# Kernel optimization log

Measured on AMD Instinct MI355X. Metric: run time of the kernel, lower is better.

Reference implementation:

```python
import jax, jax.numpy as jnp
import numpy as np

N = 50000          # nodes
E = 800000         # edges (before self-loops)
G = 64             # graphs in batch
VOCAB = 10000
EMB = 62
HEADS = 4
C = 64             # per-head channels
NUM_CLASSES = 10
NEG_SLOPE = 0.2


def setup_inputs() -> dict:
    key = jax.random.key(0)
    ks = jax.random.split(key, 24)
    inp = {}
    inp['x_ids'] = jax.random.randint(ks[0], (N,), 0, VOCAB)
    inp['degrees'] = jax.random.uniform(ks[1], (N, 2), dtype=jnp.float32)
    inp['edge_src'] = jax.random.randint(ks[2], (E,), 0, N)
    inp['edge_dst'] = jax.random.randint(ks[3], (E,), 0, N)
    inp['batch'] = jnp.sort(jax.random.randint(ks[4], (N,), 0, G))
    # parameters
    inp['emb'] = jax.random.normal(ks[5], (VOCAB, EMB), dtype=jnp.float32)
    d_in = EMB + 2  # 64
    s = lambda f: 1.0 / np.sqrt(f)
    inp['W1'] = jax.random.normal(ks[6], (HEADS * C, d_in), dtype=jnp.float32) * s(d_in)
    inp['as1'] = jax.random.normal(ks[7], (HEADS, C), dtype=jnp.float32) * s(C)
    inp['ad1'] = jax.random.normal(ks[8], (HEADS, C), dtype=jnp.float32) * s(C)
    inp['b1'] = jnp.zeros((HEADS * C,), dtype=jnp.float32)
    inp['W2'] = jax.random.normal(ks[9], (HEADS * C, HEADS * C), dtype=jnp.float32) * s(HEADS * C)
    inp['as2'] = jax.random.normal(ks[10], (HEADS, C), dtype=jnp.float32) * s(C)
    inp['ad2'] = jax.random.normal(ks[11], (HEADS, C), dtype=jnp.float32) * s(C)
    inp['b2'] = jnp.zeros((HEADS * C,), dtype=jnp.float32)
    inp['W3'] = jax.random.normal(ks[12], (1 * C, HEADS * C), dtype=jnp.float32) * s(HEADS * C)
    inp['as3'] = jax.random.normal(ks[13], (1, C), dtype=jnp.float32) * s(C)
    inp['ad3'] = jax.random.normal(ks[14], (1, C), dtype=jnp.float32) * s(C)
    inp['b3'] = jnp.zeros((C,), dtype=jnp.float32)
    inp['linW'] = jax.random.normal(ks[15], (NUM_CLASSES, C), dtype=jnp.float32) * s(C)
    inp['linb'] = jnp.zeros((NUM_CLASSES,), dtype=jnp.float32)
    return inp


def gat_conv(x, src, dst, W, att_src, att_dst, bias, heads, out_ch, concat):
    n = x.shape[0]
    h = (x @ W.T).reshape(n, heads, out_ch)              # [N,H,C]
    a_src = jnp.sum(h * att_src, axis=-1)                # [N,H]
    a_dst = jnp.sum(h * att_dst, axis=-1)                # [N,H]
    e = jax.nn.leaky_relu(a_src[src] + a_dst[dst], NEG_SLOPE)  # [E,H]
    # segmented softmax over incoming edges of each dst node
    emax = jax.ops.segment_max(e, dst, num_segments=n)
    ex = jnp.exp(e - emax[dst])
    denom = jax.ops.segment_sum(ex, dst, num_segments=n)
    alpha = ex / (denom[dst] + 1e-16)                    # [E,H]
    msg = h[src] * alpha[:, :, None]                     # [E,H,C]
    out = jax.ops.segment_sum(msg, dst, num_segments=n)  # [N,H,C]
    out = out.reshape(n, heads * out_ch) if concat else out.mean(axis=1)
    return out + bias


def reference(x_ids, degrees, edge_src, edge_dst, batch, emb,
              W1, as1, ad1, b1, W2, as2, ad2, b2, W3, as3, ad3, b3, linW, linb):
    n = x_ids.shape[0]
    # add self-loops (PyG GATConv default)
    loop = jnp.arange(n)
    src = jnp.concatenate([edge_src, loop])
    dst = jnp.concatenate([edge_dst, loop])
    x = jnp.concatenate([emb[x_ids], degrees], axis=1)   # [N, EMB+2]
    x = jax.nn.relu(gat_conv(x, src, dst, W1, as1, ad1, b1, HEADS, C, True))
    x = jax.nn.relu(gat_conv(x, src, dst, W2, as2, ad2, b2, HEADS, C, True))
    x = jax.nn.relu(gat_conv(x, src, dst, W3, as3, ad3, b3, 1, C, False))
    # global mean pool over graphs
    sums = jax.ops.segment_sum(x, batch, num_segments=G)                    # [G,C]
    cnts = jax.ops.segment_sum(jnp.ones((n,), x.dtype), batch, num_segments=G)
    pooled = sums / jnp.maximum(cnts, 1.0)[:, None]
    return pooled @ linW.T + linb                         # [G, num_classes]
```

## Files before the change

kernel.cpp:

```cpp
#include <hip/hip_runtime.h>
#include <hip/hip_bf16.h>
#include <cstdint>

#define NEG_SLOPE 0.2f

typedef __bf16 bf16x8 __attribute__((ext_vector_type(8)));
typedef float  f32x4  __attribute__((ext_vector_type(4)));

__device__ __forceinline__ unsigned short f2bf(float f) {
    unsigned int u = __float_as_uint(f);
    u += 0x7fffu + ((u >> 16) & 1u);
    return (unsigned short)(u >> 16);
}
__device__ __forceinline__ float bf2f(unsigned short u) {
    return __uint_as_float((unsigned int)u << 16);
}

__global__ void prep_kernel(const float* __restrict__ W1, int n1,
                            const float* __restrict__ W2, int n2,
                            const float* __restrict__ W3, int n3,
                            unsigned short* __restrict__ w1b, unsigned short* __restrict__ w2b,
                            unsigned short* __restrict__ w3b,
                            const int* __restrict__ ids, const float* __restrict__ degs,
                            const float* __restrict__ emb, unsigned short* __restrict__ x,
                            const int* __restrict__ edst, int* __restrict__ cnt,
                            const int* __restrict__ batch, int* __restrict__ gcnt,
                            int Nn, int E0, int E2, int G,
                            int bW, int bX, int bH)
{
    int b = blockIdx.x;
    if (b < bW) {
        int i = b * 256 + threadIdx.x;
        if (i < n1) w1b[i] = f2bf(W1[i]);
        int j = i - n1;
        if (j >= 0 && j < n2) w2b[j] = f2bf(W2[j]);
        int k = j - n2;
        if (k >= 0 && k < n3) w3b[k] = f2bf(W3[k]);
    } else if (b < bX) {
        int node = (b - bW) * 4 + (threadIdx.x >> 6);
        int lane = threadIdx.x & 63;
        if (node < Nn) {
            int id = ids[node];
            float v;
            if (lane < 62) v = emb[(size_t)id * 62 + lane];
            else           v = degs[node * 2 + (lane - 62)];
            x[(size_t)node * 64 + lane] = f2bf(v);
        }
    } else if (b < bH) {
        int e = (b - bX) * 256 + threadIdx.x;
        if (e < E2) {
            int d = (e < E0) ? edst[e] : (e - E0);
            atomicAdd(&cnt[d], 1);
        }
    } else {
        int g = threadIdx.x;
        if (g < G) {
            int lo0 = 0, hi = Nn;
            while (lo0 < hi) { int mid = (lo0 + hi) >> 1; if (batch[mid] < g) lo0 = mid + 1; else hi = mid; }
            int lo1 = lo0; hi = Nn;
            while (lo1 < hi) { int mid = (lo1 + hi) >> 1; if (batch[mid] < g + 1) lo1 = mid + 1; else hi = mid; }
            gcnt[g] = lo1 - lo0;
        }
    }
}

__global__ void scan_part_kernel(const int* __restrict__ cnt, int* __restrict__ part, int Nn)
{
    int t = threadIdx.x;
    int base = blockIdx.x * 2048 + t * 8;
    int s = 0;
    if (base + 8 <= Nn) {
        int4 a = *reinterpret_cast<const int4*>(cnt + base);
        int4 b = *reinterpret_cast<const int4*>(cnt + base + 4);
        s = a.x + a.y + a.z + a.w + b.x + b.y + b.z + b.w;
    } else {
        for (int k = 0; k < 8; ++k)
            if (base + k < Nn) s += cnt[base + k];
    }
#pragma unroll
    for (int off = 32; off >= 1; off >>= 1) s += __shfl_xor(s, off, 64);
    __shared__ int ws[4];
    int wid = t >> 6;
    if ((t & 63) == 0) ws[wid] = s;
    __syncthreads();
    if (t == 0) part[blockIdx.x] = ws[0] + ws[1] + ws[2] + ws[3];
}

__global__ void scan_top_kernel(int* __restrict__ part, int nparts)
{
    int t = threadIdx.x;
    int v = (t < nparts) ? part[t] : 0;
    int orig = v;
#pragma unroll
    for (int off = 1; off <= 32; off <<= 1) {
        int u = __shfl_up(v, off, 64);
        if (t >= off) v += u;
    }
    if (t < nparts) part[t] = v - orig;
}

__global__ void scan_down_kernel(const int* __restrict__ cnt, const int* __restrict__ part,
                                 int* __restrict__ row_off, int* __restrict__ cursor,
                                 int Nn, int total)
{
    int t = threadIdx.x;
    int base = blockIdx.x * 2048 + t * 8;
    int v[8];
    if (base + 8 <= Nn) {
        int4 a = *reinterpret_cast<const int4*>(cnt + base);
        int4 b = *reinterpret_cast<const int4*>(cnt + base + 4);
        v[0]=a.x; v[1]=a.y; v[2]=a.z; v[3]=a.w; v[4]=b.x; v[5]=b.y; v[6]=b.z; v[7]=b.w;
    } else {
#pragma unroll
        for (int k = 0; k < 8; ++k) v[k] = (base + k < Nn) ? cnt[base + k] : 0;
    }
    int tsum = 0;
#pragma unroll
    for (int k = 0; k < 8; ++k) tsum += v[k];
    int incl = tsum;
#pragma unroll
    for (int off = 1; off <= 32; off <<= 1) {
        int u = __shfl_up(incl, off, 64);
        if ((t & 63) >= off) incl += u;
    }
    int texcl = incl - tsum;
    __shared__ int ws[4];
    int wid = t >> 6;
    if ((t & 63) == 63) ws[wid] = incl;
    __syncthreads();
    int wbase = 0;
#pragma unroll
    for (int w = 0; w < 4; ++w) wbase += (w < wid) ? ws[w] : 0;
    int run = part[blockIdx.x] + wbase + texcl;

    if (base + 8 <= Nn) {
        int o[8];
#pragma unroll
        for (int k = 0; k < 8; ++k) { o[k] = run; run += v[k]; }
        *reinterpret_cast<int4*>(row_off + base)     = make_int4(o[0], o[1], o[2], o[3]);
        *reinterpret_cast<int4*>(row_off + base + 4) = make_int4(o[4], o[5], o[6], o[7]);
        *reinterpret_cast<int4*>(cursor + base)      = make_int4(o[0], o[1], o[2], o[3]);
        *reinterpret_cast<int4*>(cursor + base + 4)  = make_int4(o[4], o[5], o[6], o[7]);
    } else {
#pragma unroll
        for (int k = 0; k < 8; ++k) {
            if (base + k < Nn) {
                row_off[base + k] = run;
                cursor[base + k]  = run;
                run += v[k];
            }
        }
    }
    if (blockIdx.x == 0 && t == 0) row_off[Nn] = total;
}

__global__ void scatter_kernel(const int* __restrict__ esrc, const int* __restrict__ edst,
                               int* __restrict__ cursor, int* __restrict__ csr_src,
                               int E0, int E2)
{
    int e = blockIdx.x * blockDim.x + threadIdx.x;
    if (e >= E2) return;
    int s, d;
    if (e < E0) { s = esrc[e]; d = edst[e]; }
    else        { s = d = e - E0; }
    int pos = atomicAdd(&cursor[d], 1);
    csr_src[pos] = s;
}

__global__ void gemm_mfma(const unsigned short* __restrict__ X, const unsigned short* __restrict__ Wb,
                          unsigned short* __restrict__ Hout,
                          const float* __restrict__ aSrc, const float* __restrict__ aDst,
                          float* __restrict__ a_s, float* __restrict__ a_d,
                          int Nn, int K, int F)
{
    int wid  = (blockIdx.x * blockDim.x + threadIdx.x) >> 6;
    int lane = threadIdx.x & 63;
    int mtiles = (Nn + 63) >> 6;
    int ftiles = F >> 6;
    if (wid >= mtiles * ftiles) return;
    int ft = wid / mtiles;
    int mt = wid - ft * mtiles;
    int m0 = mt << 6, f0 = ft << 6;
    int r = lane & 15, g = lane >> 4, g4 = g << 2;

    const unsigned short* xrow[4];
#pragma unroll
    for (int ja = 0; ja < 4; ++ja) {
        int row = m0 + ja * 16 + r;
        if (row >= Nn) row = Nn - 1;
        xrow[ja] = X + (size_t)row * K + g * 8;
    }
    const unsigned short* wrow = Wb + (size_t)(f0 + r) * K + g * 8;
    const size_t wstep = (size_t)16 * K;

    f32x4 acc[4][4];
#pragma unroll
    for (int a = 0; a < 4; ++a)
#pragma unroll
        for (int b = 0; b < 4; ++b) acc[a][b] = f32x4{0.f, 0.f, 0.f, 0.f};

    for (int k0 = 0; k0 < K; k0 += 32) {
        bf16x8 av[4], bv[4];
#pragma unroll
        for (int ja = 0; ja < 4; ++ja) av[ja] = *reinterpret_cast<const bf16x8*>(xrow[ja] + k0);
#pragma unroll
        for (int jb = 0; jb < 4; ++jb) bv[jb] = *reinterpret_cast<const bf16x8*>(wrow + jb * wstep + k0);
#pragma unroll
        for (int ja = 0; ja < 4; ++ja)
#pragma unroll
            for (int jb = 0; jb < 4; ++jb)
                acc[ja][jb] = __builtin_amdgcn_mfma_f32_16x16x32_bf16(av[ja], bv[jb], acc[ja][jb], 0, 0, 0);
    }

#pragma unroll
    for (int ja = 0; ja < 4; ++ja)
#pragma unroll
        for (int q = 0; q < 4; ++q) {
            int row = m0 + ja * 16 + g4 + q;
            if (row < Nn) {
#pragma unroll
                for (int jb = 0; jb < 4; ++jb)
                    Hout[(size_t)row * F + f0 + jb * 16 + r] = f2bf(acc[ja][jb][q]);
            }
        }

    float ps[4][4], pd[4][4];
#pragma unroll
    for (int ja = 0; ja < 4; ++ja)
#pragma unroll
        for (int q = 0; q < 4; ++q) { ps[ja][q] = 0.f; pd[ja][q] = 0.f; }
#pragma unroll
    for (int jb = 0; jb < 4; ++jb) {
        float ws_ = aSrc[f0 + jb * 16 + r];
        float wd_ = aDst[f0 + jb * 16 + r];
#pragma unroll
        for (int ja = 0; ja < 4; ++ja)
#pragma unroll
            for (int q = 0; q < 4; ++q) {
                ps[ja][q] += acc[ja][jb][q] * ws_;
                pd[ja][q] += acc[ja][jb][q] * wd_;
            }
    }
#pragma unroll
    for (int off = 1; off < 16; off <<= 1)
#pragma unroll
        for (int ja = 0; ja < 4; ++ja)
#pragma unroll
            for (int q = 0; q < 4; ++q) {
                ps[ja][q] += __shfl_xor(ps[ja][q], off, 64);
                pd[ja][q] += __shfl_xor(pd[ja][q], off, 64);
            }
    if (r == 0) {
        int Hh = F >> 6;
#pragma unroll
        for (int ja = 0; ja < 4; ++ja)
#pragma unroll
            for (int q = 0; q < 4; ++q) {
                int n = m0 + ja * 16 + g4 + q;
                if (n < Nn) {
                    a_s[(size_t)n * Hh + ft] = ps[ja][q];
                    a_d[(size_t)n * Hh + ft] = pd[ja][q];
                }
            }
    }
}

template<int H>
__global__ void aggregate_kernel(const unsigned short* __restrict__ Hb,
                                 const float* __restrict__ a_s, const float* __restrict__ a_d,
                                 const int* __restrict__ row_off, const int* __restrict__ csr_src,
                                 const float* __restrict__ bias,
                                 unsigned short* __restrict__ out, int Nn)
{
    constexpr int F = H * 64;
    constexpr int VEC = F / 64;
    __shared__ int   s_sn[4][64];
    __shared__ float s_e[4][64][H];
    int w = threadIdx.x >> 6;
    int node = blockIdx.x * 4 + w;
    int lane = threadIdx.x & 63;
    if (node >= Nn) return;
    int start = row_off[node], end = row_off[node + 1];
    int deg = end - start;

    float adn[H];
#pragma unroll
    for (int h = 0; h < H; ++h) adn[h] = a_d[(size_t)node * H + h];

    if (deg <= 64) {
        bool act = lane < deg;
        int sn = act ? csr_src[start + lane] : 0;
        float v[H];
        if (H == 4) {
            const f32x4 av = *reinterpret_cast<const f32x4*>(a_s + (size_t)sn * 4);
#pragma unroll
            for (int h = 0; h < 4; ++h) {
                float t = av[h] + adn[h];
                t = (t > 0.f) ? t : NEG_SLOPE * t;
                v[h] = act ? t : -1e30f;
            }
        } else {
            float t = a_s[sn] + adn[0];
            t = (t > 0.f) ? t : NEG_SLOPE * t;
            v[0] = act ? t : -1e30f;
        }
        float m[H], e[H], s[H];
#pragma unroll
        for (int h = 0; h < H; ++h) {
            m[h] = v[h];
#pragma unroll
            for (int off = 32; off >= 1; off >>= 1)
                m[h] = fmaxf(m[h], __shfl_xor(m[h], off, 64));
        }
#pragma unroll
        for (int h = 0; h < H; ++h) {
            e[h] = act ? __expf(v[h] - m[h]) : 0.f;
            s[h] = e[h];
#pragma unroll
            for (int off = 32; off >= 1; off >>= 1)
                s[h] += __shfl_xor(s[h], off, 64);
        }

        s_sn[w][lane] = sn;
#pragma unroll
        for (int h = 0; h < H; ++h) s_e[w][lane][h] = e[h];
        asm volatile("s_waitcnt lgkmcnt(0)" ::: "memory");

        if (H == 4) {
            int half = lane >> 5, laneh = lane & 31, hd = laneh >> 3;
            float acc[8];
#pragma unroll
            for (int k = 0; k < 8; ++k) acc[k] = 0.f;
            for (int j = 0; j < deg; j += 2) {
                int idx = j + half;
                int snj = s_sn[w][idx];
                float ex = s_e[w][idx][hd];
                const uint4 u = *reinterpret_cast<const uint4*>(Hb + (size_t)snj * 256 + laneh * 8);
                acc[0] += ex * __uint_as_float(u.x << 16);
                acc[1] += ex * __uint_as_float(u.x & 0xffff0000u);
                acc[2] += ex * __uint_as_float(u.y << 16);
                acc[3] += ex * __uint_as_float(u.y & 0xffff0000u);
                acc[4] += ex * __uint_as_float(u.z << 16);
                acc[5] += ex * __uint_as_float(u.z & 0xffff0000u);
                acc[6] += ex * __uint_as_float(u.w << 16);
                acc[7] += ex * __uint_as_float(u.w & 0xffff0000u);
            }
#pragma unroll
            for (int k = 0; k < 8; ++k) acc[k] += __shfl_xor(acc[k], 32, 64);
            if (lane < 32) {
                float sh = (hd == 0) ? s[0] : (hd == 1) ? s[1] : (hd == 2) ? s[2] : s[3];
                float inv = 1.f / (sh + 1e-16f);
                unsigned int pk[4];
#pragma unroll
                for (int k = 0; k < 4; ++k) {
                    float t0 = acc[2*k]   * inv + bias[laneh * 8 + 2*k];
                    float t1 = acc[2*k+1] * inv + bias[laneh * 8 + 2*k + 1];
                    unsigned int lo = f2bf(t0 > 0.f ? t0 : 0.f);
                    unsigned int hi = f2bf(t1 > 0.f ? t1 : 0.f);
                    pk[k] = lo | (hi << 16);
                }
                *reinterpret_cast<uint4*>(out + (size_t)node * 256 + laneh * 8) =
                    make_uint4(pk[0], pk[1], pk[2], pk[3]);
            }
        } else {
            int qtr = lane >> 4, laneq = lane & 15;
            float acc[4];
#pragma unroll
            for (int k = 0; k < 4; ++k) acc[k] = 0.f;
            for (int j = 0; j < deg; j += 4) {
                int idx = j + qtr;
                int snj = s_sn[w][idx];
                float ex = s_e[w][idx][0];
                const uint2 u = *reinterpret_cast<const uint2*>(Hb + (size_t)snj * 64 + laneq * 4);
                acc[0] += ex * __uint_as_float(u.x << 16);
                acc[1] += ex * __uint_as_float(u.x & 0xffff0000u);
                acc[2] += ex * __uint_as_float(u.y << 16);
                acc[3] += ex * __uint_as_float(u.y & 0xffff0000u);
            }
#pragma unroll
            for (int k = 0; k < 4; ++k) {
                acc[k] += __shfl_xor(acc[k], 32, 64);
                acc[k] += __shfl_xor(acc[k], 16, 64);
            }
            if (lane < 16) {
                float inv = 1.f / (s[0] + 1e-16f);
                unsigned int pk[2];
#pragma unroll
                for (int k = 0; k < 2; ++k) {
                    float t0 = acc[2*k]   * inv + bias[laneq * 4 + 2*k];
                    float t1 = acc[2*k+1] * inv + bias[laneq * 4 + 2*k + 1];
                    unsigned int lo = f2bf(t0 > 0.f ? t0 : 0.f);
                    unsigned int hi = f2bf(t1 > 0.f ? t1 : 0.f);
                    pk[k] = lo | (hi << 16);
                }
                *reinterpret_cast<uint2*>(out + (size_t)node * 64 + laneq * 4) =
                    make_uint2(pk[0], pk[1]);
            }
        }
        return;
    }

    int head = (H == 1) ? 0 : (lane >> 4);
    float m[H], s[H];
#pragma unroll
    for (int h = 0; h < H; ++h) { m[h] = -1e30f; s[h] = 0.f; }
    for (int j = start + lane; j < end; j += 64) {
        int sn = csr_src[j];
#pragma unroll
        for (int h = 0; h < H; ++h) {
            float t = a_s[(size_t)sn * H + h] + adn[h];
            t = (t > 0.f) ? t : NEG_SLOPE * t;
            m[h] = fmaxf(m[h], t);
        }
    }
#pragma unroll
    for (int off = 32; off >= 1; off >>= 1)
#pragma unroll
        for (int h = 0; h < H; ++h) m[h] = fmaxf(m[h], __shfl_xor(m[h], off, 64));
    for (int j = start + lane; j < end; j += 64) {
        int sn = csr_src[j];
#pragma unroll
        for (int h = 0; h < H; ++h) {
            float t = a_s[(size_t)sn * H + h] + adn[h];
            t = (t > 0.f) ? t : NEG_SLOPE * t;
            s[h] += __expf(t - m[h]);
        }
    }
#pragma unroll
    for (int off = 32; off >= 1; off >>= 1)
#pragma unroll
        for (int h = 0; h < H; ++h) s[h] += __shfl_xor(s[h], off, 64);

    float mh, sh, adh;
    if (H == 1) { mh = m[0]; sh = s[0]; adh = adn[0]; }
    else {
        mh  = (head == 0) ? m[0]   : (head == 1) ? m[1]   : (head == 2) ? m[2]   : m[3];
        sh  = (head == 0) ? s[0]   : (head == 1) ? s[1]   : (head == 2) ? s[2]   : s[3];
        adh = (head == 0) ? adn[0] : (head == 1) ? adn[1] : (head == 2) ? adn[2] : adn[3];
    }
    float inv = 1.f / (sh + 1e-16f);
    float acc[VEC];
#pragma unroll
    for (int k = 0; k < VEC; ++k) acc[k] = 0.f;
    for (int j = start; j < end; ++j) {
        int sn = csr_src[j];
        float t = a_s[(size_t)sn * H + head] + adh;
        t = (t > 0.f) ? t : NEG_SLOPE * t;
        float ex = __expf(t - mh);
        const unsigned short* hp = Hb + (size_t)sn * F + lane * VEC;
#pragma unroll
        for (int k = 0; k < VEC; ++k) acc[k] += ex * bf2f(hp[k]);
    }
#pragma unroll
    for (int k = 0; k < VEC; ++k) {
        int f = lane * VEC + k;
        float t = acc[k] * inv + bias[f];
        out[(size_t)node * F + f] = f2bf(t > 0.f ? t : 0.f);
    }
}

__global__ void pool_kernel(const unsigned short* __restrict__ x, const int* __restrict__ batch,
                            float* __restrict__ gsums, int Nn)
{
    int lane = threadIdx.x;
    int n0 = blockIdx.x * 64;
    if (n0 >= Nn) return;
    int nend = min(n0 + 64, Nn);
    float acc = 0.f;
    int gcur = batch[n0];
    for (int n = n0; n < nend; ++n) {
        int g = batch[n];
        if (g != gcur) {
            atomicAdd(&gsums[gcur * 64 + lane], acc);
            acc = 0.f;
            gcur = g;
        }
        acc += bf2f(x[(size_t)n * 64 + lane]);
    }
    atomicAdd(&gsums[gcur * 64 + lane], acc);
}

__global__ void final_kernel(const float* __restrict__ gsums, const int* __restrict__ gcnt,
                             const float* __restrict__ linW, const float* __restrict__ linb,
                             float* __restrict__ out, int G)
{
    int t = threadIdx.x;
    if (t >= G * 10) return;
    int g = t / 10, j = t % 10;
    float cnt = (float)max(gcnt[g], 1);
    float acc = 0.f;
#pragma unroll
    for (int c = 0; c < 64; ++c) acc += gsums[g * 64 + c] * linW[j * 64 + c];
    out[g * 10 + j] = acc / cnt + linb[j];
}

extern "C" void kernel_launch(void* const* d_in, const int* in_sizes, int n_in,
                              void* d_out, int out_size, void* d_ws, size_t ws_size,
                              hipStream_t stream)
{
    const int*   x_ids    = (const int*)d_in[0];
    const float* degrees  = (const float*)d_in[1];
    const int*   edge_src = (const int*)d_in[2];
    const int*   edge_dst = (const int*)d_in[3];
    const int*   batch    = (const int*)d_in[4];
    const float* emb      = (const float*)d_in[5];
    const float* W1  = (const float*)d_in[6];
    const float* as1 = (const float*)d_in[7];
    const float* ad1 = (const float*)d_in[8];
    const float* b1  = (const float*)d_in[9];
    const float* W2  = (const float*)d_in[10];
    const float* as2 = (const float*)d_in[11];
    const float* ad2 = (const float*)d_in[12];
    const float* b2  = (const float*)d_in[13];
    const float* W3  = (const float*)d_in[14];
    const float* as3 = (const float*)d_in[15];
    const float* ad3 = (const float*)d_in[16];
    const float* b3  = (const float*)d_in[17];
    const float* linW = (const float*)d_in[18];
    const float* linb = (const float*)d_in[19];

    const int N  = in_sizes[0];
    const int E0 = in_sizes[2];
    const int E2 = E0 + N;
    const int G  = out_size / 10;
    const int nW1 = in_sizes[6], nW2 = in_sizes[10], nW3 = in_sizes[14];

    char* p = (char*)d_ws;
    size_t off = 0;
    auto take = [&](size_t bytes) {
        void* q = p + off;
        off = (off + bytes + 255) & ~(size_t)255;
        return q;
    };
    unsigned short* xA  = (unsigned short*)take((size_t)N * 256 * 2);
    unsigned short* xB  = (unsigned short*)take((size_t)N * 256 * 2);
    float* a_s     = (float*)take((size_t)N * 4 * 4);
    float* a_d     = (float*)take((size_t)N * 4 * 4);
    int*   cnt     = (int*)take((size_t)N * 4);
    int*   row_off = (int*)take((size_t)(N + 1) * 4);
    int*   cursor  = (int*)take((size_t)N * 4);
    int*   csr_src = (int*)take((size_t)E2 * 4);
    float* gsums   = (float*)take((size_t)G * 64 * 4);
    int*   gcnt    = (int*)take((size_t)G * 4);
    int*   part    = (int*)take((size_t)64 * 4);
    unsigned short* w1b = (unsigned short*)take((size_t)nW1 * 2);
    unsigned short* w2b = (unsigned short*)take((size_t)nW2 * 2);
    unsigned short* w3b = (unsigned short*)take((size_t)nW3 * 2);

    hipMemsetAsync(cnt, 0, (size_t)N * 4, stream);
    hipMemsetAsync(gsums, 0, (size_t)G * 64 * 4, stream);

    const int nodeBlocks4 = (N + 3) / 4;
    const int edgeBlocks  = (E2 + 255) / 256;
    const int scanBlocks  = (N + 2047) / 2048;

    const int nWtot = nW1 + nW2 + nW3;
    const int bW = (nWtot + 255) / 256;
    const int bX = bW + nodeBlocks4;
    const int bH = bX + edgeBlocks;
    prep_kernel<<<bH + 1, 256, 0, stream>>>(W1, nW1, W2, nW2, W3, nW3, w1b, w2b, w3b,
                                            x_ids, degrees, emb, xA,
                                            edge_dst, cnt, batch, gcnt,
                                            N, E0, E2, G, bW, bX, bH);

    scan_part_kernel<<<scanBlocks, 256, 0, stream>>>(cnt, part, N);
    scan_top_kernel<<<1, 64, 0, stream>>>(part, scanBlocks);
    scan_down_kernel<<<scanBlocks, 256, 0, stream>>>(cnt, part, row_off, cursor, N, E2);
    scatter_kernel<<<edgeBlocks, 256, 0, stream>>>(edge_src, edge_dst, cursor, csr_src, E0, E2);

    const int mtiles = (N + 63) / 64;
    auto gemmBlocks = [&](int ftiles) { return (mtiles * ftiles + 3) / 4; };

    gemm_mfma<<<gemmBlocks(4), 256, 0, stream>>>(xA, w1b, xB, as1, ad1, a_s, a_d, N, 64, 256);
    aggregate_kernel<4><<<nodeBlocks4, 256, 0, stream>>>(xB, a_s, a_d, row_off, csr_src, b1, xA, N);
    gemm_mfma<<<gemmBlocks(4), 256, 0, stream>>>(xA, w2b, xB, as2, ad2, a_s, a_d, N, 256, 256);
    aggregate_kernel<4><<<nodeBlocks4, 256, 0, stream>>>(xB, a_s, a_d, row_off, csr_src, b2, xA, N);
    gemm_mfma<<<gemmBlocks(1), 256, 0, stream>>>(xA, w3b, xB, as3, ad3, a_s, a_d, N, 256, 64);
    aggregate_kernel<1><<<nodeBlocks4, 256, 0, stream>>>(xB, a_s, a_d, row_off, csr_src, b3, xA, N);

    pool_kernel<<<(N + 63) / 64, 64, 0, stream>>>(xA, batch, gsums, N);
    final_kernel<<<1, ((G * 10 + 63) / 64) * 64, 0, stream>>>(gsums, gcnt, linW, linb, (float*)d_out, G);
}
```

Baseline: 391.8 us.

## Replace CSR build with fixed 64-slot per-node buckets plus overflow list

Drops the scan and scatter kernels. Edges are now placed directly into fixed 64-entry per-destination buckets during the counting pass, and edges past the 64th go to a global overflow list that high-degree nodes search linearly. The aggregate kernels are also reworked: each lane now loads wider chunks of features (32 bytes for 4 heads, 16 bytes for 1 head), and a packed (source, exp) pair is kept in LDS. This removes four launches and a pass over the edges, at the cost of a larger bucket buffer and a slow linear overflow scan if many nodes exceed 64 edges.

```diff
diff --git a/kernel.cpp b/kernel.cpp
--- a/kernel.cpp
+++ b/kernel.cpp
@@ -14,6 +14,10 @@
 }
 __device__ __forceinline__ float bf2f(unsigned short u) {
     return __uint_as_float((unsigned int)u << 16);
+}
+__device__ __forceinline__ void fma2(float2& a, float ex, unsigned int u) {
+    a.x = fmaf(ex, __uint_as_float(u << 16),         a.x);
+    a.y = fmaf(ex, __uint_as_float(u & 0xffff0000u), a.y);
 }
 
 __global__ void prep_kernel(const float* __restrict__ W1, int n1,
@@ -23,7 +27,9 @@
                             unsigned short* __restrict__ w3b,
                             const int* __restrict__ ids, const float* __restrict__ degs,
                             const float* __restrict__ emb, unsigned short* __restrict__ x,
-                            const int* __restrict__ edst, int* __restrict__ cnt,
+                            const int* __restrict__ esrc, const int* __restrict__ edst,
+                            int* __restrict__ cnt, int* __restrict__ bucket,
+                            int* __restrict__ ovd, int* __restrict__ ovs, int* __restrict__ n_over,
                             const int* __restrict__ batch, int* __restrict__ gcnt,
                             int Nn, int E0, int E2, int G,
                             int bW, int bX, int bH)
@@ -49,8 +55,15 @@
     } else if (b < bH) {
         int e = (b - bX) * 256 + threadIdx.x;
         if (e < E2) {
-            int d = (e < E0) ? edst[e] : (e - E0);
-            atomicAdd(&cnt[d], 1);
+            int s, d;
+            if (e < E0) { s = esrc[e]; d = edst[e]; }
+            else        { s = d = e - E0; }
+            int pos = atomicAdd(&cnt[d], 1);
+            if (pos < 64) bucket[(size_t)d * 64 + pos] = s;
+            else {
+                int o = atomicAdd(n_over, 1);
+                ovd[o] = d; ovs[o] = s;
+            }
         }
     } else {
         int g = threadIdx.x;
@@ -62,109 +75,6 @@
             gcnt[g] = lo1 - lo0;
         }
     }
-}
-
-__global__ void scan_part_kernel(const int* __restrict__ cnt, int* __restrict__ part, int Nn)
-{
-    int t = threadIdx.x;
-    int base = blockIdx.x * 2048 + t * 8;
-    int s = 0;
-    if (base + 8 <= Nn) {
-        int4 a = *reinterpret_cast<const int4*>(cnt + base);
-        int4 b = *reinterpret_cast<const int4*>(cnt + base + 4);
-        s = a.x + a.y + a.z + a.w + b.x + b.y + b.z + b.w;
-    } else {
-        for (int k = 0; k < 8; ++k)
-            if (base + k < Nn) s += cnt[base + k];
-    }
-#pragma unroll
-    for (int off = 32; off >= 1; off >>= 1) s += __shfl_xor(s, off, 64);
-    __shared__ int ws[4];
-    int wid = t >> 6;
-    if ((t & 63) == 0) ws[wid] = s;
-    __syncthreads();
-    if (t == 0) part[blockIdx.x] = ws[0] + ws[1] + ws[2] + ws[3];
-}
-
-__global__ void scan_top_kernel(int* __restrict__ part, int nparts)
-{
-    int t = threadIdx.x;
-    int v = (t < nparts) ? part[t] : 0;
-    int orig = v;
-#pragma unroll
-    for (int off = 1; off <= 32; off <<= 1) {
-        int u = __shfl_up(v, off, 64);
-        if (t >= off) v += u;
-    }
-    if (t < nparts) part[t] = v - orig;
-}
-
-__global__ void scan_down_kernel(const int* __restrict__ cnt, const int* __restrict__ part,
-                                 int* __restrict__ row_off, int* __restrict__ cursor,
-                                 int Nn, int total)
-{
-    int t = threadIdx.x;
-    int base = blockIdx.x * 2048 + t * 8;
-    int v[8];
-    if (base + 8 <= Nn) {
-        int4 a = *reinterpret_cast<const int4*>(cnt + base);
-        int4 b = *reinterpret_cast<const int4*>(cnt + base + 4);
-        v[0]=a.x; v[1]=a.y; v[2]=a.z; v[3]=a.w; v[4]=b.x; v[5]=b.y; v[6]=b.z; v[7]=b.w;
-    } else {
-#pragma unroll
-        for (int k = 0; k < 8; ++k) v[k] = (base + k < Nn) ? cnt[base + k] : 0;
-    }
-    int tsum = 0;
-#pragma unroll
-    for (int k = 0; k < 8; ++k) tsum += v[k];
-    int incl = tsum;
-#pragma unroll
-    for (int off = 1; off <= 32; off <<= 1) {
-        int u = __shfl_up(incl, off, 64);
-        if ((t & 63) >= off) incl += u;
-    }
-    int texcl = incl - tsum;
-    __shared__ int ws[4];
-    int wid = t >> 6;
-    if ((t & 63) == 63) ws[wid] = incl;
-    __syncthreads();
-    int wbase = 0;
-#pragma unroll
-    for (int w = 0; w < 4; ++w) wbase += (w < wid) ? ws[w] : 0;
-    int run = part[blockIdx.x] + wbase + texcl;
-
-    if (base + 8 <= Nn) {
-        int o[8];
-#pragma unroll
-        for (int k = 0; k < 8; ++k) { o[k] = run; run += v[k]; }
-        *reinterpret_cast<int4*>(row_off + base)     = make_int4(o[0], o[1], o[2], o[3]);
-        *reinterpret_cast<int4*>(row_off + base + 4) = make_int4(o[4], o[5], o[6], o[7]);
-        *reinterpret_cast<int4*>(cursor + base)      = make_int4(o[0], o[1], o[2], o[3]);
-        *reinterpret_cast<int4*>(cursor + base + 4)  = make_int4(o[4], o[5], o[6], o[7]);
-    } else {
-#pragma unroll
-        for (int k = 0; k < 8; ++k) {
-            if (base + k < Nn) {
-                row_off[base + k] = run;
-                cursor[base + k]  = run;
-                run += v[k];
-            }
-        }
-    }
-    if (blockIdx.x == 0 && t == 0) row_off[Nn] = total;
-}
-
-__global__ void scatter_kernel(const int* __restrict__ esrc, const int* __restrict__ edst,
-                               int* __restrict__ cursor, int* __restrict__ csr_src,
-                               int E0, int E2)
-{
-    int e = blockIdx.x * blockDim.x + threadIdx.x;
-    if (e >= E2) return;
-    int s, d;
-    if (e < E0) { s = esrc[e]; d = edst[e]; }
-    else        { s = d = e - E0; }
-    int pos = atomicAdd(&cursor[d], 1);
-    csr_src[pos] = s;
 }
 
 __global__ void gemm_mfma(const unsigned short* __restrict__ X, const unsigned short* __restrict__ Wb,
@@ -268,20 +178,20 @@
 template<int H>
 __global__ void aggregate_kernel(const unsigned short* __restrict__ Hb,
                                  const float* __restrict__ a_s, const float* __restrict__ a_d,
-                                 const int* __restrict__ row_off, const int* __restrict__ csr_src,
+                                 const int* __restrict__ cnt, const int* __restrict__ bucket,
+                                 const int* __restrict__ ovd, const int* __restrict__ ovs,
+                                 const int* __restrict__ n_over,
                                  const float* __restrict__ bias,
                                  unsigned short* __restrict__ out, int Nn)
 {
     constexpr int F = H * 64;
     constexpr int VEC = F / 64;
-    __shared__ int   s_sn[4][64];
-    __shared__ float s_e[4][64][H];
+    __shared__ uint2 s_pk[4][64][H];
     int w = threadIdx.x >> 6;
     int node = blockIdx.x * 4 + w;
     int lane = threadIdx.x & 63;
     if (node >= Nn) return;
-    int start = row_off[node], end = row_off[node + 1];
-    int deg = end - start;
+    int deg = cnt[node];
 
     float adn[H];
 #pragma unroll
@@ -289,7 +199,7 @@
 
     if (deg <= 64) {
         bool act = lane < deg;
-        int sn = act ? csr_src[start + lane] : 0;
+        int sn = act ? bucket[(size_t)node * 64 + lane] : 0;
         float v[H];
         if (H == 4) {
             const f32x4 av = *reinterpret_cast<const f32x4*>(a_s + (size_t)sn * 4);
@@ -321,91 +231,97 @@
                 s[h] += __shfl_xor(s[h], off, 64);
         }
 
-        s_sn[w][lane] = sn;
-#pragma unroll
-        for (int h = 0; h < H; ++h) s_e[w][lane][h] = e[h];
+#pragma unroll
+        for (int h = 0; h < H; ++h)
+            s_pk[w][lane][h] = make_uint2((unsigned int)sn, __float_as_uint(e[h]));
         asm volatile("s_waitcnt lgkmcnt(0)" ::: "memory");
 
         if (H == 4) {
-            int half = lane >> 5, laneh = lane & 31, hd = laneh >> 3;
-            float acc[8];
-#pragma unroll
-            for (int k = 0; k < 8; ++k) acc[k] = 0.f;
-            for (int j = 0; j < deg; j += 2) {
-                int idx = j + half;
-                int snj = s_sn[w][idx];
-                float ex = s_e[w][idx][hd];
-                const uint4 u = *reinterpret_cast<const uint4*>(Hb + (size_t)snj * 256 + laneh * 8);
-                acc[0] += ex * __uint_as_float(u.x << 16);
-                acc[1] += ex * __uint_as_float(u.x & 0xffff0000u);
-                acc[2] += ex * __uint_as_float(u.y << 16);
-                acc[3] += ex * __uint_as_float(u.y & 0xffff0000u);
-                acc[4] += ex * __uint_as_float(u.z << 16);
-                acc[5] += ex * __uint_as_float(u.z & 0xffff0000u);
-                acc[6] += ex * __uint_as_float(u.w << 16);
-                acc[7] += ex * __uint_as_float(u.w & 0xffff0000u);
-            }
-#pragma unroll
-            for (int k = 0; k < 8; ++k) acc[k] += __shfl_xor(acc[k], 32, 64);
-            if (lane < 32) {
-                float sh = (hd == 0) ? s[0] : (hd == 1) ? s[1] : (hd == 2) ? s[2] : s[3];
+            int laneq = lane & 15, qtr = lane >> 4, hd = laneq >> 2;
+            float2 acc2[8];
+#pragma unroll
+            for (int k = 0; k < 8; ++k) acc2[k] = make_float2(0.f, 0.f);
+            for (int j = 0; j < deg; j += 4) {
+                uint2 pk = s_pk[w][j + qtr][hd];
+                float ex = __uint_as_float(pk.y);
+                const uint4* hp = reinterpret_cast<const uint4*>(Hb + (size_t)pk.x * 256 + laneq * 16);
+                uint4 u0 = hp[0];
+                uint4 u1 = hp[1];
+                fma2(acc2[0], ex, u0.x); fma2(acc2[1], ex, u0.y);
+                fma2(acc2[2], ex, u0.z); fma2(acc2[3], ex, u0.w);
+                fma2(acc2[4], ex, u1.x); fma2(acc2[5], ex, u1.y);
+                fma2(acc2[6], ex, u1.z); fma2(acc2[7], ex, u1.w);
+            }
+#pragma unroll
+            for (int k = 0; k < 8; ++k) {
+                acc2[k].x += __shfl_xor(acc2[k].x, 32, 64);
+                acc2[k].y += __shfl_xor(acc2[k].y, 32, 64);
+                acc2[k].x += __shfl_xor(acc2[k].x, 16, 64);
+                acc2[k].y += __shfl_xor(acc2[k].y, 16, 64);
+            }
+            if (lane < 16) {
+                int hd2 = lane >> 2;
+                float sh = (hd2 == 0) ? s[0] : (hd2 == 1) ? s[1] : (hd2 == 2) ? s[2] : s[3];
                 float inv = 1.f / (sh + 1e-16f);
-                unsigned int pk[4];
-#pragma unroll
-                for (int k = 0; k < 4; ++k) {
-                    float t0 = acc[2*k]   * inv + bias[laneh * 8 + 2*k];
-                    float t1 = acc[2*k+1] * inv + bias[laneh * 8 + 2*k + 1];
+                unsigned int pk8[8];
+#pragma unroll
+                for (int k = 0; k < 8; ++k) {
+                    float t0 = acc2[k].x * inv + bias[lane * 16 + 2 * k];
+                    float t1 = acc2[k].y * inv + bias[lane * 16 + 2 * k + 1];
                     unsigned int lo = f2bf(t0 > 0.f ? t0 : 0.f);
                     unsigned int hi = f2bf(t1 > 0.f ? t1 : 0.f);
-                    pk[k] = lo | (hi << 16);
+                    pk8[k] = lo | (hi << 16);
                 }
-                *reinterpret_cast<uint4*>(out + (size_t)node * 256 + laneh * 8) =
-                    make_uint4(pk[0], pk[1], pk[2], pk[3]);
+                uint4* op = reinterpret_cast<uint4*>(out + (size_t)node * 256 + lane * 16);
+                op[0] = make_uint4(pk8[0], pk8[1], pk8[2], pk8[3]);
+                op[1] = make_uint4(pk8[4], pk8[5], pk8[6], pk8[7]);
             }
         } else {
-            int qtr = lane >> 4, laneq = lane & 15;
-            float acc[4];
-#pragma unroll
-            for (int k = 0; k < 4; ++k) acc[k] = 0.f;
-            for (int j = 0; j < deg; j += 4) {
-                int idx = j + qtr;
-                int snj = s_sn[w][idx];
-                float ex = s_e[w][idx][0];
-                const uint2 u = *reinterpret_cast<const uint2*>(Hb + (size_t)snj * 64 + laneq * 4);
-                acc[0] += ex * __uint_as_float(u.x << 16);
-                acc[1] += ex * __uint_as_float(u.x & 0xffff0000u);
-                acc[2] += ex * __uint_as_float(u.y << 16);
-                acc[3] += ex * __uint_as_float(u.y & 0xffff0000u);
+            int laneo = lane & 7, oct = lane >> 3;
+            float2 acc2[4];
+#pragma unroll
+            for (int k = 0; k < 4; ++k) acc2[k] = make_float2(0.f, 0.f);
+            for (int j = 0; j < deg; j += 8) {
+                uint2 pk = s_pk[w][j + oct][0];
+                float ex = __uint_as_float(pk.y);
+                const uint4 u = *reinterpret_cast<const uint4*>(Hb + (size_t)pk.x * 64 + laneo * 8);
+                fma2(acc2[0], ex, u.x); fma2(acc2[1], ex, u.y);
+                fma2(acc2[2], ex, u.z); fma2(acc2[3], ex, u.w);
             }
 #pragma unroll
             for (int k = 0; k < 4; ++k) {
-                acc[k] += __shfl_xor(acc[k], 32, 64);
-                acc[k] += __shfl_xor(acc[k], 16, 64);
-            }
-            if (lane < 16) {
+                acc2[k].x += __shfl_xor(acc2[k].x, 32, 64);
+                acc2[k].y += __shfl_xor(acc2[k].y, 32, 64);
+                acc2[k].x += __shfl_xor(acc2[k].x, 16, 64);
+                acc2[k].y += __shfl_xor(acc2[k].y, 16, 64);
+                acc2[k].x += __shfl_xor(acc2[k].x, 8, 64);
+                acc2[k].y += __shfl_xor(acc2[k].y, 8, 64);
+            }
+            if (lane < 8) {
                 float inv = 1.f / (s[0] + 1e-16f);
-                unsigned int pk[2];
-#pragma unroll
-                for (int k = 0; k < 2; ++k) {
-                    float t0 = acc[2*k]   * inv + bias[laneq * 4 + 2*k];
-                    float t1 = acc[2*k+1] * inv + bias[laneq * 4 + 2*k + 1];
+                unsigned int pk4[4];
+#pragma unroll
+                for (int k = 0; k < 4; ++k) {
+                    float t0 = acc2[k].x * inv + bias[lane * 8 + 2 * k];
+                    float t1 = acc2[k].y * inv + bias[lane * 8 + 2 * k + 1];
                     unsigned int lo = f2bf(t0 > 0.f ? t0 : 0.f);
                     unsigned int hi = f2bf(t1 > 0.f ? t1 : 0.f);
-                    pk[k] = lo | (hi << 16);
+                    pk4[k] = lo | (hi << 16);
                 }
-                *reinterpret_cast<uint2*>(out + (size_t)node * 64 + laneq * 4) =
-                    make_uint2(pk[0], pk[1]);
+                *reinterpret_cast<uint4*>(out + (size_t)node * 64 + lane * 8) =
+                    make_uint4(pk4[0], pk4[1], pk4[2], pk4[3]);
             }
         }
         return;
     }
 
+    int nov = *n_over;
     int head = (H == 1) ? 0 : (lane >> 4);
     float m[H], s[H];
 #pragma unroll
     for (int h = 0; h < H; ++h) { m[h] = -1e30f; s[h] = 0.f; }
-    for (int j = start + lane; j < end; j += 64) {
-        int sn = csr_src[j];
+    {
+        int sn = bucket[(size_t)node * 64 + lane];
 #pragma unroll
         for (int h = 0; h < H; ++h) {
             float t = a_s[(size_t)sn * H + h] + adn[h];
@@ -413,12 +329,32 @@
             m[h] = fmaxf(m[h], t);
         }
     }
+    for (int i = lane; i < nov; i += 64) {
+        if (ovd[i] != node) continue;
+        int sn = ovs[i];
+#pragma unroll
+        for (int h = 0; h < H; ++h) {
+            float t = a_s[(size_t)sn * H + h] + adn[h];
+            t = (t > 0.f) ? t : NEG_SLOPE * t;
+            m[h] = fmaxf(m[h], t);
+        }
+    }
 #pragma unroll
     for (int off = 32; off >= 1; off >>= 1)
 #pragma unroll
         for (int h = 0; h < H; ++h) m[h] = fmaxf(m[h], __shfl_xor(m[h], off, 64));
-    for (int j = start + lane; j < end; j += 64) {
-        int sn = csr_src[j];
+    {
+        int sn = bucket[(size_t)node * 64 + lane];
+#pragma unroll
+        for (int h = 0; h < H; ++h) {
+            float t = a_s[(size_t)sn * H + h] + adn[h];
+            t = (t > 0.f) ? t : NEG_SLOPE * t;
+            s[h] += __expf(t - m[h]);
+        }
+    }
+    for (int i = lane; i < nov; i += 64) {
+        if (ovd[i] != node) continue;
+        int sn = ovs[i];
 #pragma unroll
         for (int h = 0; h < H; ++h) {
             float t = a_s[(size_t)sn * H + h] + adn[h];
@@ -442,8 +378,18 @@
     float acc[VEC];
 #pragma unroll
     for (int k = 0; k < VEC; ++k) acc[k] = 0.f;
-    for (int j = start; j < end; ++j) {
-        int sn = csr_src[j];
+    for (int j = 0; j < 64; ++j) {
+        int sn = bucket[(size_t)node * 64 + j];
+        float t = a_s[(size_t)sn * H + head] + adh;
+        t = (t > 0.f) ? t : NEG_SLOPE * t;
+        float ex = __expf(t - mh);
+        const unsigned short* hp = Hb + (size_t)sn * F + lane * VEC;
+#pragma unroll
+        for (int k = 0; k < VEC; ++k) acc[k] += ex * bf2f(hp[k]);
+    }
+    for (int i = 0; i < nov; ++i) {
+        if (ovd[i] != node) continue;
+        int sn = ovs[i];
         float t = a_s[(size_t)sn * H + head] + adh;
         t = (t > 0.f) ? t : NEG_SLOPE * t;
         float ex = __expf(t - mh);
@@ -536,23 +482,22 @@
     unsigned short* xB  = (unsigned short*)take((size_t)N * 256 * 2);
     float* a_s     = (float*)take((size_t)N * 4 * 4);
     float* a_d     = (float*)take((size_t)N * 4 * 4);
-    int*   cnt     = (int*)take((size_t)N * 4);
-    int*   row_off = (int*)take((size_t)(N + 1) * 4);
-    int*   cursor  = (int*)take((size_t)N * 4);
-    int*   csr_src = (int*)take((size_t)E2 * 4);
+    int*   cnt     = (int*)take((size_t)(N + 64) * 4);
+    int*   n_over  = cnt + N;
+    int*   bucket  = (int*)take((size_t)N * 64 * 4);
+    int*   ovd     = (int*)take((size_t)E2 * 4);
+    int*   ovs     = (int*)take((size_t)E2 * 4);
     float* gsums   = (float*)take((size_t)G * 64 * 4);
     int*   gcnt    = (int*)take((size_t)G * 4);
-    int*   part    = (int*)take((size_t)64 * 4);
     unsigned short* w1b = (unsigned short*)take((size_t)nW1 * 2);
     unsigned short* w2b = (unsigned short*)take((size_t)nW2 * 2);
     unsigned short* w3b = (unsigned short*)take((size_t)nW3 * 2);
 
-    hipMemsetAsync(cnt, 0, (size_t)N * 4, stream);
+    hipMemsetAsync(cnt, 0, (size_t)(N + 1) * 4, stream);
     hipMemsetAsync(gsums, 0, (size_t)G * 64 * 4, stream);
 
     const int nodeBlocks4 = (N + 3) / 4;
     const int edgeBlocks  = (E2 + 255) / 256;
-    const int scanBlocks  = (N + 2047) / 2048;
 
     const int nWtot = nW1 + nW2 + nW3;
     const int bW = (nWtot + 255) / 256;
@@ -560,23 +505,19 @@
     const int bH = bX + edgeBlocks;
     prep_kernel<<<bH + 1, 256, 0, stream>>>(W1, nW1, W2, nW2, W3, nW3, w1b, w2b, w3b,
                                             x_ids, degrees, emb, xA,
-                                            edge_dst, cnt, batch, gcnt,
+                                            edge_src, edge_dst, cnt, bucket, ovd, ovs, n_over,
+                                            batch, gcnt,
                                             N, E0, E2, G, bW, bX, bH);
-
-    scan_part_kernel<<<scanBlocks, 256, 0, stream>>>(cnt, part, N);
-    scan_top_kernel<<<1, 64, 0, stream>>>(part, scanBlocks);
-    scan_down_kernel<<<scanBlocks, 256, 0, stream>>>(cnt, part, row_off, cursor, N, E2);
-    scatter_kernel<<<edgeBlocks, 256, 0, stream>>>(edge_src, edge_dst, cursor, csr_src, E0, E2);
 
     const int mtiles = (N + 63) / 64;
     auto gemmBlocks = [&](int ftiles) { return (mtiles * ftiles + 3) / 4; };
 
     gemm_mfma<<<gemmBlocks(4), 256, 0, stream>>>(xA, w1b, xB, as1, ad1, a_s, a_d, N, 64, 256);
-    aggregate_kernel<4><<<nodeBlocks4, 256, 0, stream>>>(xB, a_s, a_d, row_off, csr_src, b1, xA, N);
+    aggregate_kernel<4><<<nodeBlocks4, 256, 0, stream>>>(xB, a_s, a_d, cnt, bucket, ovd, ovs, n_over, b1, xA, N);
     gemm_mfma<<<gemmBlocks(4), 256, 0, stream>>>(xA, w2b, xB, as2, ad2, a_s, a_d, N, 256, 256);
-    aggregate_kernel<4><<<nodeBlocks4, 256, 0, stream>>>(xB, a_s, a_d, row_off, csr_src, b2, xA, N);
+    aggregate_kernel<4><<<nodeBlocks4, 256, 0, stream>>>(xB, a_s, a_d, cnt, bucket, ovd, ovs, n_over, b2, xA, N);
     gemm_mfma<<<gemmBlocks(1), 256, 0, stream>>>(xA, w3b, xB, as3, ad3, a_s, a_d, N, 256, 64);
-    aggregate_kernel<1><<<nodeBlocks4, 256, 0, stream>>>(xB, a_s, a_d, row_off, csr_src, b3, xA, N);
+    aggregate_kernel<1><<<nodeBlocks4, 256, 0, stream>>>(xB, a_s, a_d, cnt, bucket, ovd, ovs, n_over, b3, xA, N);
 
     pool_kernel<<<(N + 63) / 64, 64, 0, stream>>>(xA, batch, gsums, N);
     final_kernel<<<1, ((G * 10 + 63) / 64) * 64, 0, stream>>>(gsums, gcnt, linW, linb, (float*)d_out, G);
```

New measurement: 372.2 us. -5.0%, faster.
